# Optimization experiments

Measured on AMD Instinct MI355X. Metric: run time of the kernel, lower is better.

The kernel has to match this reference:

```python
import jax, jax.numpy as jnp
import numpy as np

NEG = -1000000000.0
EPS = 1e-05

def setup_inputs() -> dict:
    key = jax.random.key(0)
    k1, k2, k3, k4, k5 = jax.random.split(key, 5)
    B, L, E, Q = 64, 2048, 512, 256
    encoded_vecs = jax.random.normal(k1, (B, L, E), dtype=jnp.float32)
    query = jax.random.normal(k2, (B, Q), dtype=jnp.float32)
    length = jax.random.randint(k3, (B,), 1, L + 1, dtype=jnp.int32)
    # Xavier-normal-ish params
    W1 = jax.random.normal(k4, (E + Q, E), dtype=jnp.float32) * jnp.sqrt(2.0 / (E + Q + E))
    b1 = jnp.zeros((E,), dtype=jnp.float32)
    v = jax.random.normal(k5, (E,), dtype=jnp.float32) * jnp.sqrt(2.0 / (E + 1))
    return {"encoded_vecs": encoded_vecs, "query": query, "length": length,
            "W1": W1, "b1": b1, "v": v}

def reference(encoded_vecs, query, length, W1, b1, v):
    B, L, E = encoded_vecs.shape
    # broadcast 2D query over the length dim (repeat in torch code)
    q = jnp.broadcast_to(query[:, None, :], (B, L, query.shape[-1]))
    h = jnp.concatenate([encoded_vecs, q], axis=2)            # [B, L, E+Q]
    u = jnp.tanh(jnp.einsum('blc,ce->ble', h, W1) + b1)       # [B, L, E]
    logits = jnp.einsum('ble,e->bl', u, v)                    # [B, L]
    # masked softmax (faithful to masked_softmax in source)
    mask = (jnp.arange(L)[None, :] < length[:, None])         # [B, L] bool
    masked_logits = jnp.where(mask, logits, NEG)
    max_logits = jnp.max(masked_logits, axis=1, keepdims=True)
    exps = jnp.exp(masked_logits - max_logits) * mask.astype(logits.dtype)
    attention = exps / (jnp.sum(exps, axis=1, keepdims=True) + EPS)  # [B, L]
    context = jnp.einsum('bl,ble->be', attention, encoded_vecs)      # [B, E]
    return (context, attention)
```

## Files before the change

### kernel.cpp

```cpp
#include <hip/hip_runtime.h>

typedef __attribute__((ext_vector_type(4))) float float4v;
typedef __attribute__((ext_vector_type(2))) float float2v;
typedef __attribute__((ext_vector_type(8))) short short8;
typedef __attribute__((ext_vector_type(4))) float f32x4;

#define NEGV (-1000000000.0f)

#define MTOT (64 * 2048)

__device__ __forceinline__ unsigned short f2bf(float f) {
    unsigned int u = __float_as_uint(f);
    u += 0x7fffu + ((u >> 16) & 1u);
    return (unsigned short)(u >> 16);
}

__device__ __forceinline__ void gload_lds16(const void* g, void* l) {
    __builtin_amdgcn_global_load_lds(
        (__attribute__((address_space(1))) unsigned int*)(unsigned long long)(g),
        (__attribute__((address_space(3))) unsigned int*)(unsigned int)(unsigned long long)(l),
        16, 0, 0);
}

__global__ __launch_bounds__(256)
void prep_wt_kernel(const float* __restrict__ W1, unsigned short* __restrict__ Wt) {
    __shared__ float t[32][33];
    int bx = blockIdx.x & 15;
    int by = blockIdx.x >> 4;
    int tx = threadIdx.x & 31;
    int ty = threadIdx.x >> 5;
    #pragma unroll
    for (int i = 0; i < 4; ++i)
        t[ty + 8 * i][tx] = W1[(bx * 32 + ty + 8 * i) * 512 + by * 32 + tx];
    __syncthreads();
    #pragma unroll
    for (int i = 0; i < 4; ++i)
        Wt[(by * 32 + ty + 8 * i) * 512 + bx * 32 + tx] = f2bf(t[tx][ty + 8 * i]);
}

__global__ void prep_qc_kernel(const float* __restrict__ query, const float* __restrict__ W1,
                               const float* __restrict__ b1, float* __restrict__ qc) {
    int b = blockIdx.x;
    int e = threadIdx.x;
    float acc0 = b1[e];
    float acc1 = b1[e + 256];
    const float* w = W1 + 512 * 512;
    #pragma unroll 8
    for (int q = 0; q < 256; ++q) {
        float qv = query[b * 256 + q];
        acc0 += qv * w[q * 512 + e];
        acc1 += qv * w[q * 512 + e + 256];
    }
    qc[b * 512 + e] = acc0;
    qc[b * 512 + e + 256] = acc1;
}

__global__ void build_wl_kernel(const int* __restrict__ length, int* __restrict__ wl,
                                int* __restrict__ meta) {
    int bm = blockIdx.x * 256 + threadIdx.x;
    int b = bm >> 4;
    int l0 = (bm & 15) * 128;
    if (l0 < length[b]) {
        int idx = atomicAdd(&meta[0], 1);
        wl[idx] = bm;
    }
}

__global__ __launch_bounds__(512)
void gemm_logits_kernel(const float* __restrict__ A,
                        const unsigned short* __restrict__ Wt,
                        const float* __restrict__ qc,
                        const float* __restrict__ v,
                        const int* __restrict__ wl,
                        int* __restrict__ meta,
                        float* __restrict__ part)
{
    __shared__ unsigned short As[2 * 128 * 32];
    __shared__ unsigned short Bs[2 * 256 * 32];
    __shared__ float lred[128][4];
    __shared__ int s_t;

    int tid = threadIdx.x;
    int lane = tid & 63;
    int w = tid >> 6;
    int wm = w >> 2, wn = w & 3;

    int ar_r = tid >> 2;
    int ar_q = tid & 3;
    int awr = ar_r * 64 + ((ar_q * 16) ^ (((ar_r >> 1) & 3) << 4));
    int offw = w * 2048 + lane * 16;

    int aoff[4], boff[4];
    int kb = 16 * (lane >> 4);
    #pragma unroll
    for (int mi = 0; mi < 4; ++mi) {
        int ar = wm * 64 + (lane & 15) + mi * 16;
        aoff[mi] = ar * 64 + (kb ^ (((ar >> 1) & 3) << 4));
    }
    #pragma unroll
    for (int ni = 0; ni < 4; ++ni) {
        int br = wn * 64 + (lane & 15) + ni * 16;
        boff[ni] = br * 64 + (kb ^ (((br >> 1) & 3) << 4));
    }

    int nw = meta[0] * 2;

    for (;;) {
        if (tid == 0) s_t = atomicAdd(&meta[1], 1);
        __syncthreads();
        int t = s_t;
        if (t >= nw) break;

        int bm = wl[t >> 1];
        int bn = t & 1;
        int b = bm >> 4;
        long row0 = (long)bm * 128;
        int col0 = bn * 256;

        const char* gAr = (const char*)A + (row0 + ar_r) * 2048 + ar_q * 32;
        const char* gB0;
        const char* gB1;
        {
            int o = offw;
            int r = o >> 6;
            gB0 = (const char*)Wt + (long)(col0 + r) * 1024 + ((o & 63) ^ (((r >> 1) & 3) << 4));
            o = offw + 1024;
            r = o >> 6;
            gB1 = (const char*)Wt + (long)(col0 + r) * 1024 + ((o & 63) ^ (((r >> 1) & 3) << 4));
        }

        f32x4 acc[4][4] = {};
        float4v P0, P1;

#define GISSUE(t_, sI) do {                                                  \
    const char* ga_ = gAr + (t_) * 128;                                      \
    P0 = *(const float4v*)(ga_);                                             \
    P1 = *(const float4v*)(ga_ + 16);                                        \
    char* lb_ = (char*)Bs + (sI) * 16384 + offw;                             \
    gload_lds16(gB0 + (t_) * 64, lb_);                                       \
    gload_lds16(gB1 + (t_) * 64, lb_ + 1024);                                \
} while (0)

#define CVTW(sW) do {                                                        \
    union { unsigned int u[4]; short8 s; } pk_;                              \
    pk_.u[0] = (unsigned int)f2bf(P0[0]) | ((unsigned int)f2bf(P0[1]) << 16);\
    pk_.u[1] = (unsigned int)f2bf(P0[2]) | ((unsigned int)f2bf(P0[3]) << 16);\
    pk_.u[2] = (unsigned int)f2bf(P1[0]) | ((unsigned int)f2bf(P1[1]) << 16);\
    pk_.u[3] = (unsigned int)f2bf(P1[2]) | ((unsigned int)f2bf(P1[3]) << 16);\
    *(short8*)((char*)As + (sW) * 8192 + awr) = pk_.s;                       \
} while (0)

#define KCOMP(sC) do {                                                       \
    const char* as_ = (const char*)As + (sC) * 8192;                         \
    const char* bs_ = (const char*)Bs + (sC) * 16384;                        \
    short8 af_[4];                                                           \
    _Pragma("unroll")                                                        \
    for (int mi = 0; mi < 4; ++mi) af_[mi] = *(const short8*)(as_ + aoff[mi]); \
    _Pragma("unroll")                                                        \
    for (int ni = 0; ni < 4; ++ni) {                                         \
        short8 bf_ = *(const short8*)(bs_ + boff[ni]);                       \
        _Pragma("unroll")                                                    \
        for (int mi = 0; mi < 4; ++mi)                                       \
            acc[mi][ni] = __builtin_amdgcn_mfma_f32_16x16x32_bf16(af_[mi], bf_, acc[mi][ni], 0, 0, 0); \
    }                                                                        \
} while (0)

#define KITER(t_) do {                                                       \
    GISSUE((t_) + 1, ((t_) + 1) & 1);                                        \
    KCOMP((t_) & 1);                                                         \
    asm volatile("s_waitcnt vmcnt(2)" ::: "memory");                         \
    CVTW(((t_) + 1) & 1);                                                    \
    asm volatile("s_waitcnt vmcnt(0) lgkmcnt(0)" ::: "memory");              \
    __builtin_amdgcn_s_barrier();                                            \
    asm volatile("" ::: "memory");                                           \
} while (0)

        GISSUE(0, 0);
        asm volatile("s_waitcnt vmcnt(2)" ::: "memory");
        CVTW(0);
        asm volatile("s_waitcnt vmcnt(0) lgkmcnt(0)" ::: "memory");
        __builtin_amdgcn_s_barrier();
        asm volatile("" ::: "memory");

        KITER(0);  KITER(1);  KITER(2);  KITER(3);
        KITER(4);  KITER(5);  KITER(6);  KITER(7);
        KITER(8);  KITER(9);  KITER(10); KITER(11);
        KITER(12); KITER(13); KITER(14);
        KCOMP(1);

        const float* qcb = qc + b * 512;
        float vcol[4], qcol[4];
        #pragma unroll
        for (int ni = 0; ni < 4; ++ni) {
            int c = col0 + wn * 64 + ni * 16 + (lane & 15);
            vcol[ni] = v[c];
            qcol[ni] = qcb[c];
        }
        #pragma unroll
        for (int mi = 0; mi < 4; ++mi) {
            #pragma unroll
            for (int j2 = 0; j2 < 4; ++j2) {
                float s = 0.f;
                #pragma unroll
                for (int ni = 0; ni < 4; ++ni) {
                    float xx = acc[mi][ni][j2] + qcol[ni];
                    float e2 = __expf(2.0f * xx);
                    float tt = 1.0f - 2.0f * __builtin_amdgcn_rcpf(e2 + 1.0f);
                    s += tt * vcol[ni];
                }
                s += __shfl_xor(s, 1);
                s += __shfl_xor(s, 2);
                s += __shfl_xor(s, 4);
                s += __shfl_xor(s, 8);
                if ((lane & 15) == 0)
                    lred[wm * 64 + mi * 16 + 4 * (lane >> 4) + j2][wn] = s;
            }
        }
        __syncthreads();
        if (tid < 128) {
            float lg = lred[tid][0] + lred[tid][1] + lred[tid][2] + lred[tid][3];
            part[bn * MTOT + row0 + tid] = lg;
        }
    }
}

__global__ void softmax_kernel(const float* __restrict__ part, const int* __restrict__ length,
                               float* __restrict__ att, float* __restrict__ ctx) {
    int b = blockIdx.x;
    int len = length[b];
    int tid = threadIdx.x;
    int lane = tid & 63, wv = tid >> 6;
    const float* p0 = part + b * 2048;
    float* ab = att + b * 2048;

    ctx[b * 512 + tid] = 0.f;
    ctx[b * 512 + 256 + tid] = 0.f;

    float vals[8];
    float mymax = -3.402823466e38f;
    #pragma unroll
    for (int i = 0; i < 8; ++i) {
        int l = tid + i * 256;
        float xv = NEGV;
        if (l < len)
            xv = p0[l] + p0[MTOT + l];
        vals[i] = xv;
        mymax = fmaxf(mymax, xv);
    }
    #pragma unroll
    for (int m = 32; m; m >>= 1) mymax = fmaxf(mymax, __shfl_xor(mymax, m));
    __shared__ float sm[4];
    if (lane == 0) sm[wv] = mymax;
    __syncthreads();
    float bmax = fmaxf(fmaxf(sm[0], sm[1]), fmaxf(sm[2], sm[3]));

    float mysum = 0.f;
    #pragma unroll
    for (int i = 0; i < 8; ++i) {
        int l = tid + i * 256;
        float e = (l < len) ? __expf(vals[i] - bmax) : 0.f;
        vals[i] = e;
        mysum += e;
    }
    #pragma unroll
    for (int m = 32; m; m >>= 1) mysum += __shfl_xor(mysum, m);
    __shared__ float ss[4];
    if (lane == 0) ss[wv] = mysum;
    __syncthreads();
    float tot = ss[0] + ss[1] + ss[2] + ss[3];
    float inv = 1.0f / (tot + 1e-5f);
    #pragma unroll
    for (int i = 0; i < 8; ++i) {
        int l = tid + i * 256;
        ab[l] = vals[i] * inv;
    }
}

__global__ void ctx_kernel(const float* __restrict__ att, const float* __restrict__ enc,
                           const int* __restrict__ length, float* __restrict__ ctx) {
    int b = blockIdx.x;
    int lc = blockIdx.y;
    int len = length[b];
    int l0 = lc * 128;
    if (l0 >= len) return;
    int lim = len - l0;
    if (lim > 128) lim = 128;

    int t = threadIdx.x;
    const float* ab = att + b * 2048 + l0;
    const float* eb = enc + ((long)(b * 2048 + l0)) * 512 + t * 2;
    float c0 = 0.f, c1 = 0.f;
    #pragma unroll 4
    for (int l = 0; l < lim; ++l) {
        float a = ab[l];
        float2v e = *(const float2v*)(eb);
        eb += 512;
        c0 += a * e.x;
        c1 += a * e.y;
    }
    atomicAdd(&ctx[b * 512 + 2 * t], c0);
    atomicAdd(&ctx[b * 512 + 2 * t + 1], c1);
}

extern "C" void kernel_launch(void* const* d_in, const int* in_sizes, int n_in,
                              void* d_out, int out_size, void* d_ws, size_t ws_size,
                              hipStream_t stream) {
    const float* enc    = (const float*)d_in[0];
    const float* query  = (const float*)d_in[1];
    const int*   length = (const int*)d_in[2];
    const float* W1     = (const float*)d_in[3];
    const float* b1     = (const float*)d_in[4];
    const float* v      = (const float*)d_in[5];

    float* out = (float*)d_out;
    float* ctx = out;
    float* att = out + 64 * 512;

    char* ws = (char*)d_ws;
    float* part        = (float*)ws;
    float* qc          = (float*)(ws + 2 * MTOT * 4);
    unsigned short* Wt = (unsigned short*)(ws + 2 * MTOT * 4 + 64 * 512 * 4);
    int* wl            = (int*)(ws + 2 * MTOT * 4 + 64 * 512 * 4 + 512 * 1024);
    int* meta          = (int*)(ws + 2 * MTOT * 4 + 64 * 512 * 4 + 512 * 1024 + 4096);

    hipMemsetAsync(meta, 0, 8, stream);
    prep_wt_kernel<<<256, 256, 0, stream>>>(W1, Wt);
    prep_qc_kernel<<<64, 256, 0, stream>>>(query, W1, b1, qc);
    build_wl_kernel<<<4, 256, 0, stream>>>(length, wl, meta);

    gemm_logits_kernel<<<512, 512, 0, stream>>>(enc, Wt, qc, v, wl, meta, part);

    softmax_kernel<<<64, 256, 0, stream>>>(part, length, att, ctx);

    dim3 g3(64, 16);
    ctx_kernel<<<g3, 256, 0, stream>>>(att, enc, length, ctx);
}
```

Before: 144.5 us.

## Pre-convert encoder to bf16 and stream it directly into LDS

A new prep kernel converts the valid encoder rows to bf16 once. The GEMM then loads both operands straight into LDS with async global-to-LDS loads, using K-tiles of 64 and a three-stage buffer, instead of converting fp32 A in registers every iteration. Each wave now writes its partial logits to one of eight slices that softmax sums, which removes the shared-memory cross-wave reduction and its barrier. The context kernel reads the bf16 copy, halving its bytes but lowering the precision of the context sum. The cost is an extra pass over the encoder and more workspace.

```diff
diff --git a/kernel.cpp b/kernel.cpp
--- a/kernel.cpp
+++ b/kernel.cpp
@@ -55,19 +55,40 @@
     qc[b * 512 + e + 256] = acc1;
 }
 
+__global__ __launch_bounds__(256)
+void prep_enc_kernel(const float* __restrict__ enc, const int* __restrict__ length,
+                     unsigned short* __restrict__ Ab) {
+    int bm = blockIdx.x;
+    int b = bm >> 4;
+    if ((bm & 15) * 128 >= length[b]) return;
+    long base = (long)bm * 128 * 512;
+    const float* src = enc + base;
+    unsigned short* dst = Ab + base;
+    int tid = threadIdx.x;
+    #pragma unroll 4
+    for (int i = 0; i < 32; ++i) {
+        long idx = (long)(i * 256 + tid) * 8;
+        float4v a = *(const float4v*)(src + idx);
+        float4v c = *(const float4v*)(src + idx + 4);
+        union { unsigned short u[8]; short8 s; } o;
+        o.u[0] = f2bf(a[0]); o.u[1] = f2bf(a[1]); o.u[2] = f2bf(a[2]); o.u[3] = f2bf(a[3]);
+        o.u[4] = f2bf(c[0]); o.u[5] = f2bf(c[1]); o.u[6] = f2bf(c[2]); o.u[7] = f2bf(c[3]);
+        *(short8*)(dst + idx) = o.s;
+    }
+}
+
 __global__ void build_wl_kernel(const int* __restrict__ length, int* __restrict__ wl,
                                 int* __restrict__ meta) {
     int bm = blockIdx.x * 256 + threadIdx.x;
     int b = bm >> 4;
-    int l0 = (bm & 15) * 128;
-    if (l0 < length[b]) {
+    if ((bm & 15) * 128 < length[b]) {
         int idx = atomicAdd(&meta[0], 1);
         wl[idx] = bm;
     }
 }
 
 __global__ __launch_bounds__(512)
-void gemm_logits_kernel(const float* __restrict__ A,
+void gemm_logits_kernel(const unsigned short* __restrict__ Ab,
                         const unsigned short* __restrict__ Wt,
                         const float* __restrict__ qc,
                         const float* __restrict__ v,
@@ -75,9 +96,8 @@
                         int* __restrict__ meta,
                         float* __restrict__ part)
 {
-    __shared__ unsigned short As[2 * 128 * 32];
-    __shared__ unsigned short Bs[2 * 256 * 32];
-    __shared__ float lred[128][4];
+    __shared__ unsigned short As[3 * 128 * 64];
+    __shared__ unsigned short Bs[3 * 256 * 64];
     __shared__ int s_t;
 
     int tid = threadIdx.x;
@@ -85,22 +105,38 @@
     int w = tid >> 6;
     int wm = w >> 2, wn = w & 3;
 
-    int ar_r = tid >> 2;
-    int ar_q = tid & 3;
-    int awr = ar_r * 64 + ((ar_q * 16) ^ (((ar_r >> 1) & 3) << 4));
-    int offw = w * 2048 + lane * 16;
-
-    int aoff[4], boff[4];
-    int kb = 16 * (lane >> 4);
+    int aoffs[2], boffs[4];
+    int asrc[2], bsrc[4];
+    #pragma unroll
+    for (int i = 0; i < 2; ++i) {
+        int off = (w * 2 + i) * 1024 + lane * 16;
+        int r = off >> 7, kb = off & 127;
+        aoffs[i] = off;
+        asrc[i] = r * 1024 + (kb ^ ((r & 7) << 4));
+    }
+    #pragma unroll
+    for (int i = 0; i < 4; ++i) {
+        int off = (w * 4 + i) * 1024 + lane * 16;
+        int r = off >> 7, kb = off & 127;
+        boffs[i] = off;
+        bsrc[i] = r * 1024 + (kb ^ ((r & 7) << 4));
+    }
+
+    int aoff[4][2], boff[4][2];
+    int kbase = (lane >> 4) * 16;
     #pragma unroll
     for (int mi = 0; mi < 4; ++mi) {
         int ar = wm * 64 + (lane & 15) + mi * 16;
-        aoff[mi] = ar * 64 + (kb ^ (((ar >> 1) & 3) << 4));
+        #pragma unroll
+        for (int kk = 0; kk < 2; ++kk)
+            aoff[mi][kk] = ar * 128 + ((kk * 64 + kbase) ^ ((ar & 7) << 4));
     }
     #pragma unroll
     for (int ni = 0; ni < 4; ++ni) {
         int br = wn * 64 + (lane & 15) + ni * 16;
-        boff[ni] = br * 64 + (kb ^ (((br >> 1) & 3) << 4));
+        #pragma unroll
+        for (int kk = 0; kk < 2; ++kk)
+            boff[ni][kk] = br * 128 + ((kk * 64 + kbase) ^ ((br & 7) << 4));
     }
 
     int nw = meta[0] * 2;
@@ -110,82 +146,74 @@
         __syncthreads();
         int t = s_t;
         if (t >= nw) break;
-
         int bm = wl[t >> 1];
         int bn = t & 1;
         int b = bm >> 4;
         long row0 = (long)bm * 128;
         int col0 = bn * 256;
 
-        const char* gAr = (const char*)A + (row0 + ar_r) * 2048 + ar_q * 32;
-        const char* gB0;
-        const char* gB1;
-        {
-            int o = offw;
-            int r = o >> 6;
-            gB0 = (const char*)Wt + (long)(col0 + r) * 1024 + ((o & 63) ^ (((r >> 1) & 3) << 4));
-            o = offw + 1024;
-            r = o >> 6;
-            gB1 = (const char*)Wt + (long)(col0 + r) * 1024 + ((o & 63) ^ (((r >> 1) & 3) << 4));
-        }
+        const char* gA = (const char*)Ab + row0 * 1024;
+        const char* gB = (const char*)Wt + (long)col0 * 1024;
 
         f32x4 acc[4][4] = {};
-        float4v P0, P1;
-
-#define GISSUE(t_, sI) do {                                                  \
-    const char* ga_ = gAr + (t_) * 128;                                      \
-    P0 = *(const float4v*)(ga_);                                             \
-    P1 = *(const float4v*)(ga_ + 16);                                        \
-    char* lb_ = (char*)Bs + (sI) * 16384 + offw;                             \
-    gload_lds16(gB0 + (t_) * 64, lb_);                                       \
-    gload_lds16(gB1 + (t_) * 64, lb_ + 1024);                                \
+
+#define STAGE(t_, sI) do {                                                   \
+    char* la_ = (char*)As + (sI) * 16384;                                    \
+    char* lb_ = (char*)Bs + (sI) * 32768;                                    \
+    gload_lds16(gA + asrc[0] + (t_) * 128, la_ + aoffs[0]);                  \
+    gload_lds16(gA + asrc[1] + (t_) * 128, la_ + aoffs[1]);                  \
+    gload_lds16(gB + bsrc[0] + (t_) * 128, lb_ + boffs[0]);                  \
+    gload_lds16(gB + bsrc[1] + (t_) * 128, lb_ + boffs[1]);                  \
+    gload_lds16(gB + bsrc[2] + (t_) * 128, lb_ + boffs[2]);                  \
+    gload_lds16(gB + bsrc[3] + (t_) * 128, lb_ + boffs[3]);                  \
 } while (0)
 
-#define CVTW(sW) do {                                                        \
-    union { unsigned int u[4]; short8 s; } pk_;                              \
-    pk_.u[0] = (unsigned int)f2bf(P0[0]) | ((unsigned int)f2bf(P0[1]) << 16);\
-    pk_.u[1] = (unsigned int)f2bf(P0[2]) | ((unsigned int)f2bf(P0[3]) << 16);\
-    pk_.u[2] = (unsigned int)f2bf(P1[0]) | ((unsigned int)f2bf(P1[1]) << 16);\
-    pk_.u[3] = (unsigned int)f2bf(P1[2]) | ((unsigned int)f2bf(P1[3]) << 16);\
-    *(short8*)((char*)As + (sW) * 8192 + awr) = pk_.s;                       \
-} while (0)
-
 #define KCOMP(sC) do {                                                       \
-    const char* as_ = (const char*)As + (sC) * 8192;                         \
-    const char* bs_ = (const char*)Bs + (sC) * 16384;                        \
-    short8 af_[4];                                                           \
+    const char* as_ = (const char*)As + (sC) * 16384;                        \
+    const char* bs_ = (const char*)Bs + (sC) * 32768;                        \
     _Pragma("unroll")                                                        \
-    for (int mi = 0; mi < 4; ++mi) af_[mi] = *(const short8*)(as_ + aoff[mi]); \
-    _Pragma("unroll")                                                        \
-    for (int ni = 0; ni < 4; ++ni) {                                         \
-        short8 bf_ = *(const short8*)(bs_ + boff[ni]);                       \
+    for (int kk = 0; kk < 2; ++kk) {                                         \
+        short8 af_[4];                                                       \
         _Pragma("unroll")                                                    \
         for (int mi = 0; mi < 4; ++mi)                                       \
-            acc[mi][ni] = __builtin_amdgcn_mfma_f32_16x16x32_bf16(af_[mi], bf_, acc[mi][ni], 0, 0, 0); \
+            af_[mi] = *(const short8*)(as_ + aoff[mi][kk]);                  \
+        _Pragma("unroll")                                                    \
+        for (int ni = 0; ni < 4; ++ni) {                                     \
+            short8 bf_ = *(const short8*)(bs_ + boff[ni][kk]);               \
+            _Pragma("unroll")                                                \
+            for (int mi = 0; mi < 4; ++mi)                                   \
+                acc[mi][ni] = __builtin_amdgcn_mfma_f32_16x16x32_bf16(af_[mi], bf_, acc[mi][ni], 0, 0, 0); \
+        }                                                                    \
     }                                                                        \
 } while (0)
 
-#define KITER(t_) do {                                                       \
-    GISSUE((t_) + 1, ((t_) + 1) & 1);                                        \
-    KCOMP((t_) & 1);                                                         \
-    asm volatile("s_waitcnt vmcnt(2)" ::: "memory");                         \
-    CVTW(((t_) + 1) & 1);                                                    \
-    asm volatile("s_waitcnt vmcnt(0) lgkmcnt(0)" ::: "memory");              \
+#define KITER(t_, stg_, sI_, sC_, VM_) do {                                  \
+    STAGE(stg_, sI_);                                                        \
+    asm volatile("s_waitcnt vmcnt(" #VM_ ")" ::: "memory");                  \
     __builtin_amdgcn_s_barrier();                                            \
     asm volatile("" ::: "memory");                                           \
+    KCOMP(sC_);                                                              \
+    asm volatile("" ::: "memory");                                           \
+    __builtin_amdgcn_s_barrier();                                            \
 } while (0)
 
-        GISSUE(0, 0);
-        asm volatile("s_waitcnt vmcnt(2)" ::: "memory");
-        CVTW(0);
-        asm volatile("s_waitcnt vmcnt(0) lgkmcnt(0)" ::: "memory");
+        STAGE(0, 0);
+        STAGE(1, 1);
+        KITER(0, 2, 2, 0, 12);
+        KITER(1, 3, 0, 1, 12);
+        KITER(2, 4, 1, 2, 12);
+        KITER(3, 5, 2, 0, 12);
+        KITER(4, 6, 0, 1, 12);
+        KITER(5, 7, 1, 2, 12);
+        asm volatile("s_waitcnt vmcnt(6)" ::: "memory");
         __builtin_amdgcn_s_barrier();
         asm volatile("" ::: "memory");
-
-        KITER(0);  KITER(1);  KITER(2);  KITER(3);
-        KITER(4);  KITER(5);  KITER(6);  KITER(7);
-        KITER(8);  KITER(9);  KITER(10); KITER(11);
-        KITER(12); KITER(13); KITER(14);
+        KCOMP(0);
+        asm volatile("" ::: "memory");
+        __builtin_amdgcn_s_barrier();
+        asm volatile("s_waitcnt vmcnt(0)" ::: "memory");
+        __builtin_amdgcn_s_barrier();
+        asm volatile("" ::: "memory");
         KCOMP(1);
 
         const float* qcb = qc + b * 512;
@@ -196,6 +224,8 @@
             vcol[ni] = v[c];
             qcol[ni] = qcb[c];
         }
+        float* pslice = part + (bn * 4 + wn) * MTOT + row0;
+        int rbase = wm * 64 + 4 * (lane >> 4);
         #pragma unroll
         for (int mi = 0; mi < 4; ++mi) {
             #pragma unroll
@@ -213,13 +243,8 @@
                 s += __shfl_xor(s, 4);
                 s += __shfl_xor(s, 8);
                 if ((lane & 15) == 0)
-                    lred[wm * 64 + mi * 16 + 4 * (lane >> 4) + j2][wn] = s;
+                    pslice[rbase + mi * 16 + j2] = s;
             }
-        }
-        __syncthreads();
-        if (tid < 128) {
-            float lg = lred[tid][0] + lred[tid][1] + lred[tid][2] + lred[tid][3];
-            part[bn * MTOT + row0 + tid] = lg;
         }
     }
 }
@@ -242,8 +267,12 @@
     for (int i = 0; i < 8; ++i) {
         int l = tid + i * 256;
         float xv = NEGV;
-        if (l < len)
-            xv = p0[l] + p0[MTOT + l];
+        if (l < len) {
+            xv = 0.f;
+            #pragma unroll
+            for (int s = 0; s < 8; ++s)
+                xv += p0[s * MTOT + l];
+        }
         vals[i] = xv;
         mymax = fmaxf(mymax, xv);
     }
@@ -276,7 +305,7 @@
     }
 }
 
-__global__ void ctx_kernel(const float* __restrict__ att, const float* __restrict__ enc,
+__global__ void ctx_kernel(const float* __restrict__ att, const unsigned short* __restrict__ Ab,
                            const int* __restrict__ length, float* __restrict__ ctx) {
     int b = blockIdx.x;
     int lc = blockIdx.y;
@@ -288,15 +317,15 @@
 
     int t = threadIdx.x;
     const float* ab = att + b * 2048 + l0;
-    const float* eb = enc + ((long)(b * 2048 + l0)) * 512 + t * 2;
+    const unsigned short* eb = Ab + ((long)(b * 2048 + l0)) * 512 + t * 2;
     float c0 = 0.f, c1 = 0.f;
     #pragma unroll 4
     for (int l = 0; l < lim; ++l) {
         float a = ab[l];
-        float2v e = *(const float2v*)(eb);
+        unsigned int wv = *(const unsigned int*)(eb);
         eb += 512;
-        c0 += a * e.x;
-        c1 += a * e.y;
+        c0 += a * __uint_as_float(wv << 16);
+        c1 += a * __uint_as_float(wv & 0xffff0000u);
     }
     atomicAdd(&ctx[b * 512 + 2 * t], c0);
     atomicAdd(&ctx[b * 512 + 2 * t + 1], c1);
@@ -318,20 +347,22 @@
 
     char* ws = (char*)d_ws;
     float* part        = (float*)ws;
-    float* qc          = (float*)(ws + 2 * MTOT * 4);
-    unsigned short* Wt = (unsigned short*)(ws + 2 * MTOT * 4 + 64 * 512 * 4);
-    int* wl            = (int*)(ws + 2 * MTOT * 4 + 64 * 512 * 4 + 512 * 1024);
-    int* meta          = (int*)(ws + 2 * MTOT * 4 + 64 * 512 * 4 + 512 * 1024 + 4096);
+    float* qc          = (float*)(ws + 8L * MTOT * 4);
+    unsigned short* Wt = (unsigned short*)(ws + 8L * MTOT * 4 + 64 * 512 * 4);
+    int* wl            = (int*)(ws + 8L * MTOT * 4 + 64 * 512 * 4 + 512 * 1024);
+    int* meta          = (int*)(ws + 8L * MTOT * 4 + 64 * 512 * 4 + 512 * 1024 + 4096);
+    unsigned short* Ab = (unsigned short*)(ws + 8L * MTOT * 4 + 64 * 512 * 4 + 512 * 1024 + 8192);
 
     hipMemsetAsync(meta, 0, 8, stream);
     prep_wt_kernel<<<256, 256, 0, stream>>>(W1, Wt);
     prep_qc_kernel<<<64, 256, 0, stream>>>(query, W1, b1, qc);
     build_wl_kernel<<<4, 256, 0, stream>>>(length, wl, meta);
-
-    gemm_logits_kernel<<<512, 512, 0, stream>>>(enc, Wt, qc, v, wl, meta, part);
+    prep_enc_kernel<<<1024, 256, 0, stream>>>(enc, length, Ab);
+
+    gemm_logits_kernel<<<256, 512, 0, stream>>>(Ab, Wt, qc, v, wl, meta, part);
 
     softmax_kernel<<<64, 256, 0, stream>>>(part, length, att, ctx);
 
     dim3 g3(64, 16);
-    ctx_kernel<<<g3, 256, 0, stream>>>(att, enc, length, ctx);
-}
+    ctx_kernel<<<g3, 256, 0, stream>>>(att, Ab, length, ctx);
+}
```

After: 155.6 us. 7.7% more time.
